# Optimization experiments

Measured on AMD Instinct MI355X. Metric: run time of the kernel, lower is better.

## Reference

```python
import jax, jax.numpy as jnp
import numpy as np

KERNEL = 5
OUT_CAPS = 8
OUT_ATOMS = 32
ROUTINGS = 3


def _squash(x):
    # squash nonlinearity: (|v|^2 / (1+|v|^2)) * v/|v|, over last (atom) axis
    norm = jnp.linalg.norm(x, axis=-1, keepdims=True)
    norm_sq = norm * norm
    return (x / norm) * (norm_sq / (1.0 + norm_sq))


def setup_inputs() -> dict:
    key = jax.random.key(0)
    k1, k2, k3 = jax.random.split(key, 3)
    B, H, Wd, inC, inA = 16, 32, 32, 8, 16
    inputs = jax.random.normal(k1, (B, H, Wd, inC, inA), dtype=jnp.float32)
    # He-normal-ish conv kernel [k, k, inA, outC*outA]
    fan_in = KERNEL * KERNEL * inA
    W = jax.random.normal(k2, (KERNEL, KERNEL, inA, OUT_CAPS * OUT_ATOMS), dtype=jnp.float32) * np.sqrt(2.0 / fan_in)
    b = jnp.full((1, 1, OUT_CAPS, OUT_ATOMS), 0.1, dtype=jnp.float32)
    return {"inputs": inputs, "W": W, "b": b}


def reference(inputs, W, b):
    B, H, Wd, inC, inA = inputs.shape
    # transpose to [inC, B, H, W, inA] and fold capsules into batch for shared conv
    x = jnp.transpose(inputs, (3, 0, 1, 2, 4)).reshape(inC * B, H, Wd, inA)
    conv = jax.lax.conv_general_dilated(
        x, W, window_strides=(1, 1), padding="SAME",
        dimension_numbers=("NHWC", "HWIO", "NHWC"))
    Hp, Wp = conv.shape[1], conv.shape[2]
    # faithful to original TF reshape (row-major) of [inC*B,...] -> [B, inC, ...]
    votes = conv.reshape(B, inC, Hp, Wp, OUT_CAPS, OUT_ATOMS)
    biases = jnp.broadcast_to(b, (Hp, Wp, OUT_CAPS, OUT_ATOMS))

    logits = jnp.zeros((B, inC, Hp, Wp, OUT_CAPS), dtype=votes.dtype)
    act = None
    for _ in range(ROUTINGS):
        route = jax.nn.softmax(logits, axis=-1)  # over output capsules
        # weighted sum of votes over input capsules: [B, Hp, Wp, outC, outA]
        preact = jnp.einsum("bihwc,bihwca->bhwca", route, votes) + biases
        act = _squash(preact)
        # agreement: dot(votes, activation) over atoms -> logit update
        logits = logits + jnp.sum(votes * act[:, None], axis=-1)
    return act
```

## Files before the change

kernel.cpp:

```cpp
#include <hip/hip_runtime.h>


typedef __attribute__((ext_vector_type(2))) _Float16 f16x2;
typedef __attribute__((ext_vector_type(8))) _Float16 f16x8;
typedef __attribute__((ext_vector_type(16))) float f32x16;

union f16x8u { f16x8 v; f16x2 d[4]; unsigned short s[8]; unsigned int u32[4]; unsigned long long u[2]; };
union f16x2u { f16x2 v; unsigned int u; unsigned short s[2]; };

__device__ __forceinline__ unsigned short f2h(float x) {
  union { _Float16 h; unsigned short u; } v;
  v.h = (_Float16)x;
  return v.u;
}

template<int CTRL>
__device__ __forceinline__ float dpp_mov(float x) {
  return __builtin_bit_cast(float, __builtin_amdgcn_update_dpp(
      0, __builtin_bit_cast(int, x), CTRL, 0xF, 0xF, true));
}
__device__ __forceinline__ float sum8_dpp(float x) {
  x += dpp_mov<0xB1>(x);
  x += dpp_mov<0x4E>(x);
  x += dpp_mov<0x141>(x);
  return x;
}

__global__ __launch_bounds__(256) void wprep_kernel(
    const float* __restrict__ W, unsigned short* __restrict__ wsh) {
  int t = blockIdx.x * 256 + threadIdx.x;
  int khkw = t >> 12;
  int rem  = t & 4095;
  int ch = rem >> 4, ia = rem & 15;
  wsh[t] = f2h(W[khkw * 4096 + ia * 256 + ch]);
}

__global__ __launch_bounds__(256, 4) void capsconv_mfma_kernel(
    const float* __restrict__ inp,
    const unsigned short* __restrict__ wsh,
    const float* __restrict__ bias,
    float* __restrict__ out)
{
  __shared__ char smem[18432];
  const _Float16* wshh = (const _Float16*)wsh;

  const int tid  = threadIdx.x;
  const int wid  = tid >> 6;
  const int lane = tid & 63;
  const int sub  = lane >> 5;
  const int ln31 = lane & 31;

  const int bid = blockIdx.x;
  const int wq = bid & 3;
  const int h  = (bid >> 2) & 31;
  const int bb = bid >> 7;
  const int i_src  = bb >> 1;
  const int b_base = (bb & 1) * 8;

  for (int e = tid; e < 1920; e += 256) {
    int kh = e / 384; int r1 = e - kh * 384;
    int ii = r1 / 48; int r2 = r1 - ii * 48;
    int wl = r2 >> 2; int iaq = r2 & 3;
    int hh = h + kh - 2;
    int wsrc = wq * 8 + wl - 2;
    float4 v = make_float4(0.f, 0.f, 0.f, 0.f);
    if ((unsigned)hh < 32u && (unsigned)wsrc < 32u)
      v = *(const float4*)(inp +
          ((((size_t)(b_base + ii) * 32 + hh) * 32 + wsrc) * 8 + i_src) * 16 + iaq * 4);
    union { _Float16 hx[4]; unsigned long long u; } pkk;
    pkk.hx[0] = (_Float16)v.x; pkk.hx[1] = (_Float16)v.y;
    pkk.hx[2] = (_Float16)v.z; pkk.hx[3] = (_Float16)v.w;
    *(unsigned long long*)(smem + kh * 3200 + ii * 400 + wl * 32 + iaq * 8) = pkk.u;
  }
  __syncthreads();

  f32x16 acc[2][2];
  #pragma unroll
  for (int mt = 0; mt < 2; ++mt)
    #pragma unroll
    for (int nt = 0; nt < 2; ++nt)
      #pragma unroll
      for (int e = 0; e < 16; ++e) acc[mt][nt][e] = 0.f;

  const char* aBase = smem + (ln31 & 7) * 400 + (ln31 >> 3) * 32 + sub * 16;
  const _Float16* bBase = wshh + (wid * 64 + ln31) * 16 + sub * 8;

  #pragma unroll
  for (int kh = 0; kh < 5; ++kh) {
    #pragma unroll
    for (int kw = 0; kw < 5; ++kw) {
      f16x8 af0 = *(const f16x8*)(aBase + kh * 3200 + kw * 32);
      f16x8 af1 = *(const f16x8*)(aBase + kh * 3200 + (kw + 4) * 32);
      f16x8 bf0 = *(const f16x8*)(bBase + (size_t)(kh * 5 + kw) * 4096);
      f16x8 bf1 = *(const f16x8*)(bBase + (size_t)(kh * 5 + kw) * 4096 + 512);
      acc[0][0] = __builtin_amdgcn_mfma_f32_32x32x16_f16(af0, bf0, acc[0][0], 0, 0, 0);
      acc[0][1] = __builtin_amdgcn_mfma_f32_32x32x16_f16(af0, bf1, acc[0][1], 0, 0, 0);
      acc[1][0] = __builtin_amdgcn_mfma_f32_32x32x16_f16(af1, bf0, acc[1][0], 0, 0, 0);
      acc[1][1] = __builtin_amdgcn_mfma_f32_32x32x16_f16(af1, bf1, acc[1][1], 0, 0, 0);
    }
  }

  float vv[2][4][8];
  {
    const int ch0 = wid * 64 + ln31;
    char* base0 = smem + (ch0 >> 2) * 72 + (ch0 & 3) * 16 + sub * 8;
    const int ch1 = ch0 + 32;
    char* base1 = smem + (ch1 >> 2) * 72 + (ch1 & 3) * 16 + sub * 8;
    #pragma unroll
    for (int mt = 0; mt < 2; ++mt) {
      __syncthreads();
      #pragma unroll
      for (int q = 0; q < 4; ++q) {
        f16x2u lo0, hi0, lo1, hi1;
        lo0.v = f16x2{(_Float16)acc[mt][0][q * 4 + 0], (_Float16)acc[mt][0][q * 4 + 1]};
        hi0.v = f16x2{(_Float16)acc[mt][0][q * 4 + 2], (_Float16)acc[mt][0][q * 4 + 3]};
        lo1.v = f16x2{(_Float16)acc[mt][1][q * 4 + 0], (_Float16)acc[mt][1][q * 4 + 1]};
        hi1.v = f16x2{(_Float16)acc[mt][1][q * 4 + 2], (_Float16)acc[mt][1][q * 4 + 3]};
        *(unsigned long long*)(base0 + q * 4608) =
            (unsigned long long)lo0.u | ((unsigned long long)hi0.u << 32);
        *(unsigned long long*)(base1 + q * 4608) =
            (unsigned long long)lo1.u | ((unsigned long long)hi1.u << 32);
      }
      __syncthreads();
      #pragma unroll
      for (int j = 0; j < 4; ++j) {
        f16x8u t8;
        t8.v = *(const f16x8*)(smem + wid * 4608 + lane * 72 + j * 16);
        #pragma unroll
        for (int ii = 0; ii < 8; ++ii) vv[mt][j][ii] = (float)t8.v[ii];
      }
    }
  }

  const int k = lane & 7;
  const float4 bv4 = *(const float4*)(bias + lane * 4);
  const float bvj[4] = {bv4.x, bv4.y, bv4.z, bv4.w};

  float logit_k[2] = {0.f, 0.f};
  float pre[2][4], scale[2] = {0.f, 0.f};

  #pragma unroll
  for (int rt = 0; rt < 3; ++rt) {
    #pragma unroll
    for (int p = 0; p < 2; ++p) {
      float r[8];
      if (rt == 0) {
        #pragma unroll
        for (int i = 0; i < 8; ++i) r[i] = 0.125f;
      } else {
        float mx = logit_k[p];
        mx = fmaxf(mx, dpp_mov<0x128>(mx));
        mx = fmaxf(mx, __shfl_xor(mx, 16, 64));
        mx = fmaxf(mx, __shfl_xor(mx, 32, 64));
        float e = __expf(logit_k[p] - mx);
        float den = e;
        den += dpp_mov<0x128>(den);
        den += __shfl_xor(den, 16, 64);
        den += __shfl_xor(den, 32, 64);
        float route_k = e / den;
        int cbase = lane & 56;
        #pragma unroll
        for (int i = 0; i < 8; ++i) r[i] = __shfl(route_k, cbase | i, 64);
      }
      #pragma unroll
      for (int j = 0; j < 4; ++j) {
        float pp = bvj[j];
        #pragma unroll
        for (int ii = 0; ii < 8; ++ii) pp = fmaf(r[ii], vv[p][j][ii], pp);
        pre[p][j] = pp;
      }
      float nsq = pre[p][0] * pre[p][0] + pre[p][1] * pre[p][1] +
                  pre[p][2] * pre[p][2] + pre[p][3] * pre[p][3];
      nsq = sum8_dpp(nsq);
      scale[p] = sqrtf(nsq) / (1.f + nsq);
      if (rt < 2) {
        float dot8[8];
        #pragma unroll
        for (int ii = 0; ii < 8; ++ii) {
          float d = vv[p][0][ii] * pre[p][0];
          d = fmaf(vv[p][1][ii], pre[p][1], d);
          d = fmaf(vv[p][2][ii], pre[p][2], d);
          d = fmaf(vv[p][3][ii], pre[p][3], d);
          dot8[ii] = sum8_dpp(d);
        }
        bool b0 = (k & 1), b1 = (k & 2), b2 = (k & 4);
        float e0 = b0 ? dot8[1] : dot8[0];
        float e1 = b0 ? dot8[3] : dot8[2];
        float e2 = b0 ? dot8[5] : dot8[4];
        float e3 = b0 ? dot8[7] : dot8[6];
        float f0 = b1 ? e1 : e0;
        float f1 = b1 ? e3 : e2;
        logit_k[p] = fmaf(scale[p], b2 ? f1 : f0, logit_k[p]);
      }
    }
  }
  const size_t base8 = (size_t)((bb * 32 + h) * 32 + wq * 8);
  #pragma unroll
  for (int p = 0; p < 2; ++p) {
    float4 o = make_float4(pre[p][0] * scale[p], pre[p][1] * scale[p],
                           pre[p][2] * scale[p], pre[p][3] * scale[p]);
    *(float4*)(out + (base8 + wid + 4 * p) * 256 + lane * 4) = o;
  }
}

extern "C" void kernel_launch(void* const* d_in, const int* in_sizes, int n_in,
                              void* d_out, int out_size, void* d_ws, size_t ws_size,
                              hipStream_t stream) {
  (void)in_sizes; (void)n_in; (void)ws_size; (void)out_size;
  const float* inp  = (const float*)d_in[0];
  const float* W    = (const float*)d_in[1];
  const float* bv   = (const float*)d_in[2];
  float* out        = (float*)d_out;
  unsigned short* wsh = (unsigned short*)d_ws;

  hipLaunchKernelGGL(wprep_kernel, dim3(400), dim3(256), 0, stream, W, wsh);
  hipLaunchKernelGGL(capsconv_mfma_kernel, dim3(2048), dim3(256), 0, stream,
                     inp, wsh, bv, out);
}
```

Measured before the change: 49.72 us.

## Pre-pad and convert input to fp16 in a prep kernel, read A operands from global

Adds a separate kernel that transposes, zero-pads and converts the input to a padded fp16 layout in workspace. The main kernel then loads MFMA A fragments straight from global/L2 instead of staging a per-block halo tile in shared memory, which removes the staging loop and one barrier. The cost is an extra kernel launch, an extra round trip through global memory for the whole input, and uncoalesced, redundant global reads for the A fragments in the inner loop.

After: 76.75 us. 54.4% more time.

```diff
diff --git a/kernel.cpp b/kernel.cpp
--- a/kernel.cpp
+++ b/kernel.cpp
@@ -35,8 +35,31 @@
   wsh[t] = f2h(W[khkw * 4096 + ia * 256 + ch]);
 }
 
+__global__ __launch_bounds__(256) void xprep_kernel(
+    const float* __restrict__ inp, _Float16* __restrict__ xt) {
+  int idx = blockIdx.x * 256 + threadIdx.x;
+  int pos = idx >> 2, iaq = idx & 3;
+  int n  = pos / 1296;
+  int r  = pos - n * 1296;
+  int hp = r / 36;
+  int wp = r - hp * 36;
+  int bb = n >> 3, ii = n & 7;
+  int b_src = (bb & 1) * 8 + ii, i_src = bb >> 1;
+  int hh = hp - 2, ww = wp - 2;
+  unsigned long long u = 0ull;
+  if ((unsigned)hh < 32u && (unsigned)ww < 32u) {
+    float4 v = *(const float4*)(inp +
+        ((((size_t)b_src * 32 + hh) * 32 + ww) * 8 + i_src) * 16 + iaq * 4);
+    union { _Float16 hx[4]; unsigned long long uu; } pk;
+    pk.hx[0] = (_Float16)v.x; pk.hx[1] = (_Float16)v.y;
+    pk.hx[2] = (_Float16)v.z; pk.hx[3] = (_Float16)v.w;
+    u = pk.uu;
+  }
+  *(unsigned long long*)(xt + (size_t)pos * 16 + iaq * 4) = u;
+}
+
 __global__ __launch_bounds__(256, 4) void capsconv_mfma_kernel(
-    const float* __restrict__ inp,
+    const _Float16* __restrict__ xt,
     const unsigned short* __restrict__ wsh,
     const float* __restrict__ bias,
     float* __restrict__ out)
@@ -54,25 +77,6 @@
   const int wq = bid & 3;
   const int h  = (bid >> 2) & 31;
   const int bb = bid >> 7;
-  const int i_src  = bb >> 1;
-  const int b_base = (bb & 1) * 8;
-
-  for (int e = tid; e < 1920; e += 256) {
-    int kh = e / 384; int r1 = e - kh * 384;
-    int ii = r1 / 48; int r2 = r1 - ii * 48;
-    int wl = r2 >> 2; int iaq = r2 & 3;
-    int hh = h + kh - 2;
-    int wsrc = wq * 8 + wl - 2;
-    float4 v = make_float4(0.f, 0.f, 0.f, 0.f);
-    if ((unsigned)hh < 32u && (unsigned)wsrc < 32u)
-      v = *(const float4*)(inp +
-          ((((size_t)(b_base + ii) * 32 + hh) * 32 + wsrc) * 8 + i_src) * 16 + iaq * 4);
-    union { _Float16 hx[4]; unsigned long long u; } pkk;
-    pkk.hx[0] = (_Float16)v.x; pkk.hx[1] = (_Float16)v.y;
-    pkk.hx[2] = (_Float16)v.z; pkk.hx[3] = (_Float16)v.w;
-    *(unsigned long long*)(smem + kh * 3200 + ii * 400 + wl * 32 + iaq * 8) = pkk.u;
-  }
-  __syncthreads();
 
   f32x16 acc[2][2];
   #pragma unroll
@@ -82,15 +86,17 @@
       #pragma unroll
       for (int e = 0; e < 16; ++e) acc[mt][nt][e] = 0.f;
 
-  const char* aBase = smem + (ln31 & 7) * 400 + (ln31 >> 3) * 32 + sub * 16;
+  const _Float16* aBase = xt +
+      (((size_t)(bb * 8 + (ln31 & 7)) * 36 + h) * 36 + wq * 8 + (ln31 >> 3)) * 16 + sub * 8;
   const _Float16* bBase = wshh + (wid * 64 + ln31) * 16 + sub * 8;
 
   #pragma unroll
   for (int kh = 0; kh < 5; ++kh) {
+    const _Float16* aK = aBase + kh * 576;
     #pragma unroll
     for (int kw = 0; kw < 5; ++kw) {
-      f16x8 af0 = *(const f16x8*)(aBase + kh * 3200 + kw * 32);
-      f16x8 af1 = *(const f16x8*)(aBase + kh * 3200 + (kw + 4) * 32);
+      f16x8 af0 = *(const f16x8*)(aK + kw * 16);
+      f16x8 af1 = *(const f16x8*)(aK + (kw + 4) * 16);
       f16x8 bf0 = *(const f16x8*)(bBase + (size_t)(kh * 5 + kw) * 4096);
       f16x8 bf1 = *(const f16x8*)(bBase + (size_t)(kh * 5 + kw) * 4096 + 512);
       acc[0][0] = __builtin_amdgcn_mfma_f32_32x32x16_f16(af0, bf0, acc[0][0], 0, 0, 0);
@@ -108,7 +114,7 @@
     char* base1 = smem + (ch1 >> 2) * 72 + (ch1 & 3) * 16 + sub * 8;
     #pragma unroll
     for (int mt = 0; mt < 2; ++mt) {
-      __syncthreads();
+      if (mt) __syncthreads();
       #pragma unroll
       for (int q = 0; q < 4; ++q) {
         f16x2u lo0, hi0, lo1, hi1;
@@ -212,8 +218,10 @@
   const float* bv   = (const float*)d_in[2];
   float* out        = (float*)d_out;
   unsigned short* wsh = (unsigned short*)d_ws;
+  _Float16* xt = (_Float16*)((char*)d_ws + 204800);
 
   hipLaunchKernelGGL(wprep_kernel, dim3(400), dim3(256), 0, stream, W, wsh);
+  hipLaunchKernelGGL(xprep_kernel, dim3(2592), dim3(256), 0, stream, inp, xt);
   hipLaunchKernelGGL(capsconv_mfma_kernel, dim3(2048), dim3(256), 0, stream,
-                     inp, wsh, bv, out);
-}
+                     xt, wsh, bv, out);
+}
```
